# Optimization experiments

Hardware: AMD Instinct MI355X
Metric: run time of the kernel (lower is better)

Reference implementation:

```python
import jax, jax.numpy as jnp
import numpy as np

B, X_DIM, Z_DIM, K = 16384, 784, 64, 64
LOG2PI = 1.8378770664093453


def setup_inputs() -> dict:
    key = jax.random.key(0)
    ks = jax.random.split(key, 8)
    pi_raw = jax.random.uniform(ks[1], (B, K), dtype=jnp.float32) + 1e-3
    pi = pi_raw / jnp.sum(pi_raw, axis=1, keepdims=True)
    return {
        "x": jax.random.normal(ks[0], (B, X_DIM), dtype=jnp.float32),
        "pi": pi,
        "qz_mu": jax.random.normal(ks[2], (B, Z_DIM), dtype=jnp.float32),
        "qz_logsigma": 0.5 * jax.random.normal(ks[3], (B, Z_DIM), dtype=jnp.float32),
        "eps": jax.random.normal(ks[4], (B, Z_DIM), dtype=jnp.float32),
        "pz_y_mu": jax.random.normal(ks[5], (K, Z_DIM), dtype=jnp.float32),
        "pz_y_logsigma": jnp.zeros((K, Z_DIM), dtype=jnp.float32),  # log(init_sigma=1.0)
        "W_dec": jax.random.normal(ks[6], (Z_DIM, X_DIM), dtype=jnp.float32) / np.sqrt(Z_DIM),
        "b_dec": jnp.zeros((X_DIM,), dtype=jnp.float32),
    }


def reference(x, pi, qz_mu, qz_logsigma, eps, pz_y_mu, pz_y_logsigma, W_dec, b_dec):
    # GMMVAE.elbo with num_samples=1; rsample reparameterized with fixed eps.
    qs = jnp.exp(qz_logsigma)                      # [B, z]
    z = qz_mu + qs * eps                           # [B, z]

    # log p(x | z): unit-variance Gaussian likelihood with linear decoder
    mean = z @ W_dec + b_dec                       # [B, x]
    log_px_z = jnp.sum(-0.5 * (x - mean) ** 2 - 0.5 * LOG2PI)

    # py_z: vectorized over all k components (fuses the original Python loop)
    ps = jnp.exp(pz_y_logsigma)                    # [k, z]
    diff = z[:, None, :] - pz_y_mu[None, :, :]     # [B, k, z]
    comp_lp = jnp.sum(-0.5 * (diff / ps[None]) ** 2 - pz_y_logsigma[None] - 0.5 * LOG2PI, axis=-1)  # [B, k]
    log_pi = jnp.log(pi)
    pzy = comp_lp + log_pi                         # [B, k]
    log_py_z = pzy - jax.scipy.special.logsumexp(pzy, axis=1, keepdims=True)
    probs = jnp.exp(log_py_z)                      # [B, k]

    # kl_y = sum_b KL(Cat(py_z) || Cat(pi))
    kl_y = jnp.sum(probs * (log_py_z - log_pi))

    # kl_z = sum_b sum_k probs[b,k] * KL(N(qz_mu, qs) || N(mu_k, ps_k)).sum(z)
    mdiff = qz_mu[:, None, :] - pz_y_mu[None, :, :]  # [B, k, z]
    klz_bk = jnp.sum(
        pz_y_logsigma[None] - qz_logsigma[:, None, :]
        + (qs[:, None, :] ** 2 + mdiff ** 2) / (2.0 * ps[None] ** 2)
        - 0.5,
        axis=-1,
    )                                              # [B, k]
    kl_z = jnp.sum(probs * klz_bk)

    elbo = (log_px_z - kl_y - kl_z) / x.shape[0]
    return elbo
```

## Files before the change

### kernel.cpp

```cpp
#include <hip/hip_runtime.h>

#define NB 16384
#define XD 784
#define ZD 64
#define KK 64
#define LOG2PI_F 1.8378770664093453f
#define LDA 72

typedef __attribute__((ext_vector_type(8))) short short8;
typedef __attribute__((ext_vector_type(4))) float floatx4;


__device__ __forceinline__ float wave_sum(float x) {
    #pragma unroll
    for (int o = 32; o > 0; o >>= 1) x += __shfl_xor(x, o, 64);
    return x;
}

__device__ __forceinline__ unsigned short f2bf(float f) {
    unsigned u = __float_as_uint(f);
    unsigned r = (u + 0x7FFF + ((u >> 16) & 1)) >> 16;
    return (unsigned short)r;
}

__device__ __forceinline__ unsigned int pack2(float a, float b) {
    return (unsigned int)f2bf(a) | ((unsigned int)f2bf(b) << 16);
}

__global__ __launch_bounds__(256) void prep_kernel(
    const float* __restrict__ W, unsigned short* __restrict__ Wt)
{
    int idx = blockIdx.x * 256 + threadIdx.x;
    if (idx < ZD * XD) {
        int k = idx / XD;
        int n = idx - k * XD;
        Wt[n * ZD + k] = f2bf(W[idx]);
    }
}

__global__ __launch_bounds__(256) void mixture_mfma_kernel(
    const float* __restrict__ pi, const float* __restrict__ qmu,
    const float* __restrict__ qls, const float* __restrict__ eps,
    const float* __restrict__ pmu_g, const float* __restrict__ plog_g,
    float* __restrict__ kly_p, float* __restrict__ klz_p)
{
    __shared__ unsigned short Az2[64 * LDA];
    __shared__ unsigned short Azm[64 * LDA];
    __shared__ unsigned short Aq2[64 * LDA];
    __shared__ unsigned short Aqm[64 * LDA];
    __shared__ unsigned short Bi2[64 * LDA];
    __shared__ unsigned short Bm1[64 * LDA];
    __shared__ float Ck_s[KK], Sk_s[KK], Gk_s[KK], sq_s[64];
    __shared__ float r1[4], r2[4];

    const int tid  = threadIdx.x;
    const int row0 = blockIdx.x * 64;

    {
        const int r  = tid >> 2;
        const int q  = tid & 3;
        const int v0 = q * 16;
        const int gb = (row0 + r) * 64 + v0;
        float4 mu4[4], ls4[4], ep4[4];
        #pragma unroll
        for (int i = 0; i < 4; ++i) {
            mu4[i] = *(const float4*)&qmu[gb + 4 * i];
            ls4[i] = *(const float4*)&qls[gb + 4 * i];
            ep4[i] = *(const float4*)&eps[gb + 4 * i];
        }
        float sls = 0.f;
        unsigned int* pz2 = (unsigned int*)&Az2[r * LDA + v0];
        unsigned int* pzm = (unsigned int*)&Azm[r * LDA + v0];
        unsigned int* pq2 = (unsigned int*)&Aq2[r * LDA + v0];
        unsigned int* pqm = (unsigned int*)&Aqm[r * LDA + v0];
        #pragma unroll
        for (int i = 0; i < 4; ++i) {
            float m0[4] = {mu4[i].x, mu4[i].y, mu4[i].z, mu4[i].w};
            float l0[4] = {ls4[i].x, ls4[i].y, ls4[i].z, ls4[i].w};
            float e0[4] = {ep4[i].x, ep4[i].y, ep4[i].z, ep4[i].w};
            float z[4], q2[4];
            #pragma unroll
            for (int j = 0; j < 4; ++j) {
                float qs = __expf(l0[j]);
                z[j]  = fmaf(qs, e0[j], m0[j]);
                q2[j] = fmaf(m0[j], m0[j], qs * qs);
                sls += l0[j];
            }
            pz2[i * 2 + 0] = pack2(z[0] * z[0], z[1] * z[1]);
            pz2[i * 2 + 1] = pack2(z[2] * z[2], z[3] * z[3]);
            pzm[i * 2 + 0] = pack2(-2.f * z[0], -2.f * z[1]);
            pzm[i * 2 + 1] = pack2(-2.f * z[2], -2.f * z[3]);
            pq2[i * 2 + 0] = pack2(q2[0], q2[1]);
            pq2[i * 2 + 1] = pack2(q2[2], q2[3]);
            pqm[i * 2 + 0] = pack2(-2.f * m0[0], -2.f * m0[1]);
            pqm[i * 2 + 1] = pack2(-2.f * m0[2], -2.f * m0[3]);
        }
        sls += __shfl_xor(sls, 1, 64);
        sls += __shfl_xor(sls, 2, 64);
        if (q == 0) sq_s[r] = sls;
    }

    {
        const int k  = tid >> 2;
        const int q  = tid & 3;
        const int v0 = q * 16;
        const int gb = k * 64 + v0;
        float s = 0.f, g = 0.f;
        unsigned int* pi2 = (unsigned int*)&Bi2[k * LDA + v0];
        unsigned int* pm1 = (unsigned int*)&Bm1[k * LDA + v0];
        #pragma unroll
        for (int i = 0; i < 4; ++i) {
            float4 mu4 = *(const float4*)&pmu_g[gb + 4 * i];
            float4 lg4 = *(const float4*)&plog_g[gb + 4 * i];
            float m0[4] = {mu4.x, mu4.y, mu4.z, mu4.w};
            float l0[4] = {lg4.x, lg4.y, lg4.z, lg4.w};
            float i2v[4], m1v[4];
            #pragma unroll
            for (int j = 0; j < 4; ++j) {
                float i2 = 0.5f * __expf(-2.f * l0[j]);
                i2v[j] = i2;
                m1v[j] = m0[j] * i2;
                g = fmaf(m0[j] * m0[j], i2, g);
                s += l0[j];
            }
            pi2[i * 2 + 0] = pack2(i2v[0], i2v[1]);
            pi2[i * 2 + 1] = pack2(i2v[2], i2v[3]);
            pm1[i * 2 + 0] = pack2(m1v[0], m1v[1]);
            pm1[i * 2 + 1] = pack2(m1v[2], m1v[3]);
        }
        s += __shfl_xor(s, 1, 64);
        s += __shfl_xor(s, 2, 64);
        g += __shfl_xor(g, 1, 64);
        g += __shfl_xor(g, 2, 64);
        if (q == 0) {
            Sk_s[k] = s;
            Gk_s[k] = g;
            Ck_s[k] = -s - 32.0f * LOG2PI_F;
        }
    }
    __syncthreads();

    const int lane  = tid & 63;
    const int wid   = tid >> 6;
    const int mm    = lane & 15;
    const int quad  = lane >> 4;
    const int rbase = wid * 16;

    const short8 az2_0 = *(const short8*)&Az2[(rbase + mm) * LDA + quad * 8];
    const short8 az2_1 = *(const short8*)&Az2[(rbase + mm) * LDA + 32 + quad * 8];
    const short8 azm_0 = *(const short8*)&Azm[(rbase + mm) * LDA + quad * 8];
    const short8 azm_1 = *(const short8*)&Azm[(rbase + mm) * LDA + 32 + quad * 8];
    const short8 aq2_0 = *(const short8*)&Aq2[(rbase + mm) * LDA + quad * 8];
    const short8 aq2_1 = *(const short8*)&Aq2[(rbase + mm) * LDA + 32 + quad * 8];
    const short8 aqm_0 = *(const short8*)&Aqm[(rbase + mm) * LDA + quad * 8];
    const short8 aqm_1 = *(const short8*)&Aqm[(rbase + mm) * LDA + 32 + quad * 8];

    floatx4 acc_a[4], acc_c[4];
    #pragma unroll
    for (int t = 0; t < 4; ++t) {
        const int kr = t * 16 + mm;
        const short8 bi0 = *(const short8*)&Bi2[kr * LDA + quad * 8];
        const short8 bi1 = *(const short8*)&Bi2[kr * LDA + 32 + quad * 8];
        const short8 bm0 = *(const short8*)&Bm1[kr * LDA + quad * 8];
        const short8 bm1 = *(const short8*)&Bm1[kr * LDA + 32 + quad * 8];
        floatx4 ca = {0.f, 0.f, 0.f, 0.f};
        ca = __builtin_amdgcn_mfma_f32_16x16x32_bf16(az2_0, bi0, ca, 0, 0, 0);
        ca = __builtin_amdgcn_mfma_f32_16x16x32_bf16(az2_1, bi1, ca, 0, 0, 0);
        ca = __builtin_amdgcn_mfma_f32_16x16x32_bf16(azm_0, bm0, ca, 0, 0, 0);
        ca = __builtin_amdgcn_mfma_f32_16x16x32_bf16(azm_1, bm1, ca, 0, 0, 0);
        acc_a[t] = ca;
        floatx4 cc = {0.f, 0.f, 0.f, 0.f};
        cc = __builtin_amdgcn_mfma_f32_16x16x32_bf16(aq2_0, bi0, cc, 0, 0, 0);
        cc = __builtin_amdgcn_mfma_f32_16x16x32_bf16(aq2_1, bi1, cc, 0, 0, 0);
        cc = __builtin_amdgcn_mfma_f32_16x16x32_bf16(aqm_0, bm0, cc, 0, 0, 0);
        cc = __builtin_amdgcn_mfma_f32_16x16x32_bf16(aqm_1, bm1, cc, 0, 0, 0);
        acc_c[t] = cc;
    }

    float comp[4][4], pz[4][4];
    #pragma unroll
    for (int t = 0; t < 4; ++t) {
        const int k = t * 16 + mm;
        const float ck = Ck_s[k], gk = Gk_s[k];
        #pragma unroll
        for (int r = 0; r < 4; ++r) {
            const int gb = row0 + rbase + quad * 4 + r;
            comp[t][r] = ck - (acc_a[t][r] + gk);
            pz[t][r] = comp[t][r] + __logf(pi[gb * 64 + k]);
        }
    }

    float kly = 0.f, klz = 0.f;
    #pragma unroll
    for (int r = 0; r < 4; ++r) {
        float mx = fmaxf(fmaxf(pz[0][r], pz[1][r]), fmaxf(pz[2][r], pz[3][r]));
        #pragma unroll
        for (int o = 1; o <= 8; o <<= 1) mx = fmaxf(mx, __shfl_xor(mx, o, 64));
        float e[4];
        float s = 0.f;
        #pragma unroll
        for (int t = 0; t < 4; ++t) { e[t] = __expf(pz[t][r] - mx); s += e[t]; }
        #pragma unroll
        for (int o = 1; o <= 8; o <<= 1) s += __shfl_xor(s, o, 64);
        const float lse = mx + __logf(s);
        const float inv = __frcp_rn(s);
        const float sql = sq_s[rbase + quad * 4 + r];
        #pragma unroll
        for (int t = 0; t < 4; ++t) {
            const int k = t * 16 + mm;
            const float p = e[t] * inv;
            kly = fmaf(p, comp[t][r] - lse, kly);
            const float cv = acc_c[t][r] + Gk_s[k];
            klz = fmaf(p, Sk_s[k] - sql + cv - 32.0f, klz);
        }
    }

    kly = wave_sum(kly);
    klz = wave_sum(klz);
    if (lane == 0) { r1[wid] = kly; r2[wid] = klz; }
    __syncthreads();
    if (tid == 0) {
        kly_p[blockIdx.x] = r1[0] + r1[1] + r1[2] + r1[3];
        klz_p[blockIdx.x] = r2[0] + r2[1] + r2[2] + r2[3];
    }
}

__global__ __launch_bounds__(256) void decoder_mfma_kernel(
    const float* __restrict__ x, const float* __restrict__ qmu,
    const float* __restrict__ qls, const float* __restrict__ eps,
    const unsigned short* __restrict__ Wt, const float* __restrict__ bd,
    float* __restrict__ dec_p)
{
    __shared__ unsigned short zt[16 * 64];
    __shared__ float rs[4];
    const int tid  = threadIdx.x;
    const int row0 = blockIdx.x * 16;

    for (int i = tid; i < 16 * 64; i += 256) {
        int g = row0 * 64 + i;
        float z = fmaf(__expf(qls[g]), eps[g], qmu[g]);
        zt[i] = f2bf(z);
    }
    __syncthreads();

    const int lane = tid & 63;
    const int wid  = tid >> 6;
    const int m    = lane & 15;
    const int quad = lane >> 4;

    const short8 af0 = *(const short8*)&zt[m * 64 + quad * 8];
    const short8 af1 = *(const short8*)&zt[m * 64 + 32 + quad * 8];

    const int xrow = (row0 + quad * 4) * XD;

    float xa0, xa1, xa2, xa3, bb;
    short8 w0, w1;
    {
        const int col = wid * 16 + m;
        xa0 = x[xrow + 0 * XD + col];
        xa1 = x[xrow + 1 * XD + col];
        xa2 = x[xrow + 2 * XD + col];
        xa3 = x[xrow + 3 * XD + col];
        bb  = bd[col];
        w0  = *(const short8*)&Wt[col * 64 + quad * 8];
        w1  = *(const short8*)&Wt[col * 64 + 32 + quad * 8];
    }

    float accl = 0.f;
    #pragma unroll 1
    for (int t = wid; t < 49; t += 4) {
        const float cx0 = xa0, cx1 = xa1, cx2 = xa2, cx3 = xa3, cb = bb;
        const short8 cw0 = w0, cw1 = w1;
        const int tn = t + 4;
        if (tn < 49) {
            const int col = tn * 16 + m;
            xa0 = x[xrow + 0 * XD + col];
            xa1 = x[xrow + 1 * XD + col];
            xa2 = x[xrow + 2 * XD + col];
            xa3 = x[xrow + 3 * XD + col];
            bb  = bd[col];
            w0  = *(const short8*)&Wt[col * 64 + quad * 8];
            w1  = *(const short8*)&Wt[col * 64 + 32 + quad * 8];
        }
        floatx4 c = {0.f, 0.f, 0.f, 0.f};
        c = __builtin_amdgcn_mfma_f32_16x16x32_bf16(af0, cw0, c, 0, 0, 0);
        c = __builtin_amdgcn_mfma_f32_16x16x32_bf16(af1, cw1, c, 0, 0, 0);
        float d0 = cx0 - (c[0] + cb);
        float d1 = cx1 - (c[1] + cb);
        float d2 = cx2 - (c[2] + cb);
        float d3 = cx3 - (c[3] + cb);
        accl = fmaf(d0, d0, accl);
        accl = fmaf(d1, d1, accl);
        accl = fmaf(d2, d2, accl);
        accl = fmaf(d3, d3, accl);
    }

    float s = wave_sum(accl);
    if (lane == 0) rs[wid] = s;
    __syncthreads();
    if (tid == 0)
        dec_p[blockIdx.x] = -0.5f * (rs[0] + rs[1] + rs[2] + rs[3]);
}

__global__ __launch_bounds__(256) void finalize_kernel(
    const float* __restrict__ dec_p, const float* __restrict__ kly_p,
    const float* __restrict__ klz_p, float* __restrict__ out)
{
    __shared__ double s0[256], s1[256], s2[256];
    const int tid = threadIdx.x;
    double a0 = 0.0, a1 = 0.0, a2 = 0.0;
    for (int i = tid; i < 1024; i += 256) a0 += (double)dec_p[i];
    a1 = (double)kly_p[tid];
    a2 = (double)klz_p[tid];
    s0[tid] = a0; s1[tid] = a1; s2[tid] = a2;
    __syncthreads();
    #pragma unroll
    for (int off = 128; off > 0; off >>= 1) {
        if (tid < off) {
            s0[tid] += s0[tid + off];
            s1[tid] += s1[tid + off];
            s2[tid] += s2[tid + off];
        }
        __syncthreads();
    }
    if (tid == 0) {
        double lpx = s0[0] - 0.5 * 1.8378770664093453 * (double)NB * (double)XD;
        out[0] = (float)((lpx - s1[0] - s2[0]) / (double)NB);
    }
}

extern "C" void kernel_launch(void* const* d_in, const int* in_sizes, int n_in,
                              void* d_out, int out_size, void* d_ws, size_t ws_size,
                              hipStream_t stream) {
    const float* x    = (const float*)d_in[0];
    const float* pi   = (const float*)d_in[1];
    const float* qmu  = (const float*)d_in[2];
    const float* qls  = (const float*)d_in[3];
    const float* eps  = (const float*)d_in[4];
    const float* pmu  = (const float*)d_in[5];
    const float* plog = (const float*)d_in[6];
    const float* W    = (const float*)d_in[7];
    const float* bd   = (const float*)d_in[8];
    float* out = (float*)d_out;

    unsigned short* Wt = (unsigned short*)d_ws;
    float* fp    = (float*)((char*)d_ws + 100352);
    float* dec_p = fp;
    float* kly_p = fp + 1024;
    float* klz_p = fp + 1280;

    prep_kernel<<<(ZD * XD + 255) / 256, 256, 0, stream>>>(W, Wt);
    mixture_mfma_kernel<<<NB / 64, 256, 0, stream>>>(pi, qmu, qls, eps, pmu, plog, kly_p, klz_p);
    decoder_mfma_kernel<<<NB / 16, 256, 0, stream>>>(x, qmu, qls, eps, Wt, bd, dec_p);
    finalize_kernel<<<1, 256, 0, stream>>>(dec_p, kly_p, klz_p, out);
}
```

Before: 127.4 us.

## Fuse mixture KL and decoder kernels into one 16-row-per-block kernel

Merges the mixture (KL) kernel and the decoder likelihood kernel into a single kernel that processes 16 rows per block. The z, q and mu operands are computed once and shared through LDS, which avoids reloading qmu, qls and eps and saves a launch. Per-component prior terms are now precomputed once in prep_kernel and read from global memory, instead of being recomputed by every block. Each wave now handles 16 components, so the logsumexp is combined across waves through shared memory, which adds a barrier and extra exp calls.

```diff
diff --git a/kernel.cpp b/kernel.cpp
--- a/kernel.cpp
+++ b/kernel.cpp
@@ -28,86 +28,27 @@
 }
 
 __global__ __launch_bounds__(256) void prep_kernel(
-    const float* __restrict__ W, unsigned short* __restrict__ Wt)
+    const float* __restrict__ W, const float* __restrict__ pmu_g,
+    const float* __restrict__ plog_g,
+    unsigned short* __restrict__ Wt, unsigned short* __restrict__ Bi2_g,
+    unsigned short* __restrict__ Bm1_g, float* __restrict__ Sk_g,
+    float* __restrict__ Gk_g, float* __restrict__ Ck_g)
 {
-    int idx = blockIdx.x * 256 + threadIdx.x;
-    if (idx < ZD * XD) {
+    const int tid = threadIdx.x;
+    const int b = blockIdx.x;
+    if (b < 196) {
+        int idx = b * 256 + tid;
         int k = idx / XD;
         int n = idx - k * XD;
         Wt[n * ZD + k] = f2bf(W[idx]);
-    }
-}
-
-__global__ __launch_bounds__(256) void mixture_mfma_kernel(
-    const float* __restrict__ pi, const float* __restrict__ qmu,
-    const float* __restrict__ qls, const float* __restrict__ eps,
-    const float* __restrict__ pmu_g, const float* __restrict__ plog_g,
-    float* __restrict__ kly_p, float* __restrict__ klz_p)
-{
-    __shared__ unsigned short Az2[64 * LDA];
-    __shared__ unsigned short Azm[64 * LDA];
-    __shared__ unsigned short Aq2[64 * LDA];
-    __shared__ unsigned short Aqm[64 * LDA];
-    __shared__ unsigned short Bi2[64 * LDA];
-    __shared__ unsigned short Bm1[64 * LDA];
-    __shared__ float Ck_s[KK], Sk_s[KK], Gk_s[KK], sq_s[64];
-    __shared__ float r1[4], r2[4];
-
-    const int tid  = threadIdx.x;
-    const int row0 = blockIdx.x * 64;
-
-    {
-        const int r  = tid >> 2;
-        const int q  = tid & 3;
-        const int v0 = q * 16;
-        const int gb = (row0 + r) * 64 + v0;
-        float4 mu4[4], ls4[4], ep4[4];
-        #pragma unroll
-        for (int i = 0; i < 4; ++i) {
-            mu4[i] = *(const float4*)&qmu[gb + 4 * i];
-            ls4[i] = *(const float4*)&qls[gb + 4 * i];
-            ep4[i] = *(const float4*)&eps[gb + 4 * i];
-        }
-        float sls = 0.f;
-        unsigned int* pz2 = (unsigned int*)&Az2[r * LDA + v0];
-        unsigned int* pzm = (unsigned int*)&Azm[r * LDA + v0];
-        unsigned int* pq2 = (unsigned int*)&Aq2[r * LDA + v0];
-        unsigned int* pqm = (unsigned int*)&Aqm[r * LDA + v0];
-        #pragma unroll
-        for (int i = 0; i < 4; ++i) {
-            float m0[4] = {mu4[i].x, mu4[i].y, mu4[i].z, mu4[i].w};
-            float l0[4] = {ls4[i].x, ls4[i].y, ls4[i].z, ls4[i].w};
-            float e0[4] = {ep4[i].x, ep4[i].y, ep4[i].z, ep4[i].w};
-            float z[4], q2[4];
-            #pragma unroll
-            for (int j = 0; j < 4; ++j) {
-                float qs = __expf(l0[j]);
-                z[j]  = fmaf(qs, e0[j], m0[j]);
-                q2[j] = fmaf(m0[j], m0[j], qs * qs);
-                sls += l0[j];
-            }
-            pz2[i * 2 + 0] = pack2(z[0] * z[0], z[1] * z[1]);
-            pz2[i * 2 + 1] = pack2(z[2] * z[2], z[3] * z[3]);
-            pzm[i * 2 + 0] = pack2(-2.f * z[0], -2.f * z[1]);
-            pzm[i * 2 + 1] = pack2(-2.f * z[2], -2.f * z[3]);
-            pq2[i * 2 + 0] = pack2(q2[0], q2[1]);
-            pq2[i * 2 + 1] = pack2(q2[2], q2[3]);
-            pqm[i * 2 + 0] = pack2(-2.f * m0[0], -2.f * m0[1]);
-            pqm[i * 2 + 1] = pack2(-2.f * m0[2], -2.f * m0[3]);
-        }
-        sls += __shfl_xor(sls, 1, 64);
-        sls += __shfl_xor(sls, 2, 64);
-        if (q == 0) sq_s[r] = sls;
-    }
-
-    {
-        const int k  = tid >> 2;
-        const int q  = tid & 3;
+    } else {
+        const int k = tid >> 2;
+        const int q = tid & 3;
         const int v0 = q * 16;
         const int gb = k * 64 + v0;
         float s = 0.f, g = 0.f;
-        unsigned int* pi2 = (unsigned int*)&Bi2[k * LDA + v0];
-        unsigned int* pm1 = (unsigned int*)&Bm1[k * LDA + v0];
+        unsigned int* pi2 = (unsigned int*)&Bi2_g[k * 64 + v0];
+        unsigned int* pm1 = (unsigned int*)&Bm1_g[k * 64 + v0];
         #pragma unroll
         for (int i = 0; i < 4; ++i) {
             float4 mu4 = *(const float4*)&pmu_g[gb + 4 * i];
@@ -133,130 +74,155 @@
         g += __shfl_xor(g, 1, 64);
         g += __shfl_xor(g, 2, 64);
         if (q == 0) {
-            Sk_s[k] = s;
-            Gk_s[k] = g;
-            Ck_s[k] = -s - 32.0f * LOG2PI_F;
+            Sk_g[k] = s;
+            Gk_g[k] = g;
+            Ck_g[k] = -s - 32.0f * LOG2PI_F;
+        }
+    }
+}
+
+__global__ __launch_bounds__(256) void fused_kernel(
+    const float* __restrict__ x, const float* __restrict__ pi,
+    const float* __restrict__ qmu, const float* __restrict__ qls,
+    const float* __restrict__ eps,
+    const unsigned short* __restrict__ Wt, const float* __restrict__ bd,
+    const unsigned short* __restrict__ Bi2_g, const unsigned short* __restrict__ Bm1_g,
+    const float* __restrict__ Sk_g, const float* __restrict__ Gk_g,
+    const float* __restrict__ Ck_g,
+    float* __restrict__ dec_p, float* __restrict__ kly_p, float* __restrict__ klz_p)
+{
+    __shared__ unsigned short Az[16 * LDA];
+    __shared__ unsigned short Az2[16 * LDA];
+    __shared__ unsigned short Azm[16 * LDA];
+    __shared__ unsigned short Aq2[16 * LDA];
+    __shared__ unsigned short Aqm[16 * LDA];
+    __shared__ float Sk_s[64], Gk_s[64], Ck_s[64], sql_s[16];
+    __shared__ float MxP[4][16], SxP[4][16];
+    __shared__ float r1[4], r2[4], rs[4];
+
+    const int tid = threadIdx.x;
+    const int row0 = blockIdx.x * 16;
+
+    {
+        const int r = tid >> 4;
+        const int c = (tid & 15) * 4;
+        const int gb = (row0 + r) * 64 + c;
+        float4 mu4 = *(const float4*)&qmu[gb];
+        float4 ls4 = *(const float4*)&qls[gb];
+        float4 ep4 = *(const float4*)&eps[gb];
+        float m0[4] = {mu4.x, mu4.y, mu4.z, mu4.w};
+        float l0[4] = {ls4.x, ls4.y, ls4.z, ls4.w};
+        float e0[4] = {ep4.x, ep4.y, ep4.z, ep4.w};
+        float z[4], q2[4], sls = 0.f;
+        #pragma unroll
+        for (int j = 0; j < 4; ++j) {
+            float qs = __expf(l0[j]);
+            z[j] = fmaf(qs, e0[j], m0[j]);
+            q2[j] = fmaf(m0[j], m0[j], qs * qs);
+            sls += l0[j];
+        }
+        unsigned* pa = (unsigned*)&Az[r * LDA + c];
+        pa[0] = pack2(z[0], z[1]);               pa[1] = pack2(z[2], z[3]);
+        unsigned* pb = (unsigned*)&Az2[r * LDA + c];
+        pb[0] = pack2(z[0] * z[0], z[1] * z[1]); pb[1] = pack2(z[2] * z[2], z[3] * z[3]);
+        unsigned* pc = (unsigned*)&Azm[r * LDA + c];
+        pc[0] = pack2(-2.f * z[0], -2.f * z[1]); pc[1] = pack2(-2.f * z[2], -2.f * z[3]);
+        unsigned* pd = (unsigned*)&Aq2[r * LDA + c];
+        pd[0] = pack2(q2[0], q2[1]);             pd[1] = pack2(q2[2], q2[3]);
+        unsigned* pe = (unsigned*)&Aqm[r * LDA + c];
+        pe[0] = pack2(-2.f * m0[0], -2.f * m0[1]); pe[1] = pack2(-2.f * m0[2], -2.f * m0[3]);
+        sls += __shfl_xor(sls, 1, 64);
+        sls += __shfl_xor(sls, 2, 64);
+        sls += __shfl_xor(sls, 4, 64);
+        sls += __shfl_xor(sls, 8, 64);
+        if ((tid & 15) == 0) sql_s[r] = sls;
+        if (tid < 64) {
+            Sk_s[tid] = Sk_g[tid];
+            Gk_s[tid] = Gk_g[tid];
+            Ck_s[tid] = Ck_g[tid];
         }
     }
     __syncthreads();
 
-    const int lane  = tid & 63;
-    const int wid   = tid >> 6;
-    const int mm    = lane & 15;
-    const int quad  = lane >> 4;
-    const int rbase = wid * 16;
-
-    const short8 az2_0 = *(const short8*)&Az2[(rbase + mm) * LDA + quad * 8];
-    const short8 az2_1 = *(const short8*)&Az2[(rbase + mm) * LDA + 32 + quad * 8];
-    const short8 azm_0 = *(const short8*)&Azm[(rbase + mm) * LDA + quad * 8];
-    const short8 azm_1 = *(const short8*)&Azm[(rbase + mm) * LDA + 32 + quad * 8];
-    const short8 aq2_0 = *(const short8*)&Aq2[(rbase + mm) * LDA + quad * 8];
-    const short8 aq2_1 = *(const short8*)&Aq2[(rbase + mm) * LDA + 32 + quad * 8];
-    const short8 aqm_0 = *(const short8*)&Aqm[(rbase + mm) * LDA + quad * 8];
-    const short8 aqm_1 = *(const short8*)&Aqm[(rbase + mm) * LDA + 32 + quad * 8];
-
-    floatx4 acc_a[4], acc_c[4];
-    #pragma unroll
-    for (int t = 0; t < 4; ++t) {
-        const int kr = t * 16 + mm;
-        const short8 bi0 = *(const short8*)&Bi2[kr * LDA + quad * 8];
-        const short8 bi1 = *(const short8*)&Bi2[kr * LDA + 32 + quad * 8];
-        const short8 bm0 = *(const short8*)&Bm1[kr * LDA + quad * 8];
-        const short8 bm1 = *(const short8*)&Bm1[kr * LDA + 32 + quad * 8];
-        floatx4 ca = {0.f, 0.f, 0.f, 0.f};
+    const int lane = tid & 63;
+    const int w    = tid >> 6;
+    const int m    = lane & 15;
+    const int quad = lane >> 4;
+    const int kk   = w * 16 + m;
+
+    floatx4 ca = {0.f, 0.f, 0.f, 0.f}, cc = {0.f, 0.f, 0.f, 0.f};
+    {
+        const short8 az2_0 = *(const short8*)&Az2[m * LDA + quad * 8];
+        const short8 az2_1 = *(const short8*)&Az2[m * LDA + 32 + quad * 8];
+        const short8 azm_0 = *(const short8*)&Azm[m * LDA + quad * 8];
+        const short8 azm_1 = *(const short8*)&Azm[m * LDA + 32 + quad * 8];
+        const short8 aq2_0 = *(const short8*)&Aq2[m * LDA + quad * 8];
+        const short8 aq2_1 = *(const short8*)&Aq2[m * LDA + 32 + quad * 8];
+        const short8 aqm_0 = *(const short8*)&Aqm[m * LDA + quad * 8];
+        const short8 aqm_1 = *(const short8*)&Aqm[m * LDA + 32 + quad * 8];
+        const short8 bi0 = *(const short8*)&Bi2_g[kk * 64 + quad * 8];
+        const short8 bi1 = *(const short8*)&Bi2_g[kk * 64 + 32 + quad * 8];
+        const short8 bm0 = *(const short8*)&Bm1_g[kk * 64 + quad * 8];
+        const short8 bm1 = *(const short8*)&Bm1_g[kk * 64 + 32 + quad * 8];
         ca = __builtin_amdgcn_mfma_f32_16x16x32_bf16(az2_0, bi0, ca, 0, 0, 0);
         ca = __builtin_amdgcn_mfma_f32_16x16x32_bf16(az2_1, bi1, ca, 0, 0, 0);
         ca = __builtin_amdgcn_mfma_f32_16x16x32_bf16(azm_0, bm0, ca, 0, 0, 0);
         ca = __builtin_amdgcn_mfma_f32_16x16x32_bf16(azm_1, bm1, ca, 0, 0, 0);
-        acc_a[t] = ca;
-        floatx4 cc = {0.f, 0.f, 0.f, 0.f};
         cc = __builtin_amdgcn_mfma_f32_16x16x32_bf16(aq2_0, bi0, cc, 0, 0, 0);
         cc = __builtin_amdgcn_mfma_f32_16x16x32_bf16(aq2_1, bi1, cc, 0, 0, 0);
         cc = __builtin_amdgcn_mfma_f32_16x16x32_bf16(aqm_0, bm0, cc, 0, 0, 0);
         cc = __builtin_amdgcn_mfma_f32_16x16x32_bf16(aqm_1, bm1, cc, 0, 0, 0);
-        acc_c[t] = cc;
-    }
-
-    float comp[4][4], pz[4][4];
+    }
+
+    const float ckv = Ck_s[kk], gkv = Gk_s[kk], skv = Sk_s[kk];
+    float comp[4], ev[4], mxw[4], sw[4];
     #pragma unroll
-    for (int t = 0; t < 4; ++t) {
-        const int k = t * 16 + mm;
-        const float ck = Ck_s[k], gk = Gk_s[k];
+    for (int r = 0; r < 4; ++r) {
+        comp[r] = ckv - (ca[r] + gkv);
+        float pzv = comp[r] + __logf(pi[(row0 + quad * 4 + r) * 64 + kk]);
+        float mx = pzv;
+        #pragma unroll
+        for (int o = 1; o <= 8; o <<= 1) mx = fmaxf(mx, __shfl_xor(mx, o, 64));
+        float e = __expf(pzv - mx);
+        float s = e;
+        #pragma unroll
+        for (int o = 1; o <= 8; o <<= 1) s += __shfl_xor(s, o, 64);
+        mxw[r] = mx; sw[r] = s; ev[r] = e;
+    }
+    if (m == 0) {
         #pragma unroll
         for (int r = 0; r < 4; ++r) {
-            const int gb = row0 + rbase + quad * 4 + r;
-            comp[t][r] = ck - (acc_a[t][r] + gk);
-            pz[t][r] = comp[t][r] + __logf(pi[gb * 64 + k]);
-        }
-    }
+            MxP[w][quad * 4 + r] = mxw[r];
+            SxP[w][quad * 4 + r] = sw[r];
+        }
+    }
+    __syncthreads();
 
     float kly = 0.f, klz = 0.f;
     #pragma unroll
     for (int r = 0; r < 4; ++r) {
-        float mx = fmaxf(fmaxf(pz[0][r], pz[1][r]), fmaxf(pz[2][r], pz[3][r]));
-        #pragma unroll
-        for (int o = 1; o <= 8; o <<= 1) mx = fmaxf(mx, __shfl_xor(mx, o, 64));
-        float e[4];
-        float s = 0.f;
-        #pragma unroll
-        for (int t = 0; t < 4; ++t) { e[t] = __expf(pz[t][r] - mx); s += e[t]; }
-        #pragma unroll
-        for (int o = 1; o <= 8; o <<= 1) s += __shfl_xor(s, o, 64);
-        const float lse = mx + __logf(s);
-        const float inv = __frcp_rn(s);
-        const float sql = sq_s[rbase + quad * 4 + r];
-        #pragma unroll
-        for (int t = 0; t < 4; ++t) {
-            const int k = t * 16 + mm;
-            const float p = e[t] * inv;
-            kly = fmaf(p, comp[t][r] - lse, kly);
-            const float cv = acc_c[t][r] + Gk_s[k];
-            klz = fmaf(p, Sk_s[k] - sql + cv - 32.0f, klz);
-        }
-    }
-
+        const int row = quad * 4 + r;
+        float g0 = MxP[0][row], g1 = MxP[1][row], g2 = MxP[2][row], g3 = MxP[3][row];
+        float gmx = fmaxf(fmaxf(g0, g1), fmaxf(g2, g3));
+        float st = SxP[0][row] * __expf(g0 - gmx) + SxP[1][row] * __expf(g1 - gmx)
+                 + SxP[2][row] * __expf(g2 - gmx) + SxP[3][row] * __expf(g3 - gmx);
+        float lse = gmx + __logf(st);
+        float p = ev[r] * __expf(mxw[r] - gmx) * __frcp_rn(st);
+        kly = fmaf(p, comp[r] - lse, kly);
+        klz = fmaf(p, skv - sql_s[row] + cc[r] + gkv - 32.0f, klz);
+    }
     kly = wave_sum(kly);
     klz = wave_sum(klz);
-    if (lane == 0) { r1[wid] = kly; r2[wid] = klz; }
-    __syncthreads();
-    if (tid == 0) {
-        kly_p[blockIdx.x] = r1[0] + r1[1] + r1[2] + r1[3];
-        klz_p[blockIdx.x] = r2[0] + r2[1] + r2[2] + r2[3];
-    }
-}
-
-__global__ __launch_bounds__(256) void decoder_mfma_kernel(
-    const float* __restrict__ x, const float* __restrict__ qmu,
-    const float* __restrict__ qls, const float* __restrict__ eps,
-    const unsigned short* __restrict__ Wt, const float* __restrict__ bd,
-    float* __restrict__ dec_p)
-{
-    __shared__ unsigned short zt[16 * 64];
-    __shared__ float rs[4];
-    const int tid  = threadIdx.x;
-    const int row0 = blockIdx.x * 16;
-
-    for (int i = tid; i < 16 * 64; i += 256) {
-        int g = row0 * 64 + i;
-        float z = fmaf(__expf(qls[g]), eps[g], qmu[g]);
-        zt[i] = f2bf(z);
-    }
-    __syncthreads();
-
-    const int lane = tid & 63;
-    const int wid  = tid >> 6;
-    const int m    = lane & 15;
-    const int quad = lane >> 4;
-
-    const short8 af0 = *(const short8*)&zt[m * 64 + quad * 8];
-    const short8 af1 = *(const short8*)&zt[m * 64 + 32 + quad * 8];
-
+    if (lane == 0) { r1[w] = kly; r2[w] = klz; }
+
+    const short8 af0 = *(const short8*)&Az[m * LDA + quad * 8];
+    const short8 af1 = *(const short8*)&Az[m * LDA + 32 + quad * 8];
     const int xrow = (row0 + quad * 4) * XD;
 
     float xa0, xa1, xa2, xa3, bb;
     short8 w0, w1;
     {
-        const int col = wid * 16 + m;
+        const int col = w * 16 + m;
         xa0 = x[xrow + 0 * XD + col];
         xa1 = x[xrow + 1 * XD + col];
         xa2 = x[xrow + 2 * XD + col];
@@ -268,7 +234,7 @@
 
     float accl = 0.f;
     #pragma unroll 1
-    for (int t = wid; t < 49; t += 4) {
+    for (int t = w; t < 49; t += 4) {
         const float cx0 = xa0, cx1 = xa1, cx2 = xa2, cx3 = xa3, cb = bb;
         const short8 cw0 = w0, cw1 = w1;
         const int tn = t + 4;
@@ -295,11 +261,14 @@
         accl = fmaf(d3, d3, accl);
     }
 
-    float s = wave_sum(accl);
-    if (lane == 0) rs[wid] = s;
+    float sdec = wave_sum(accl);
+    if (lane == 0) rs[w] = sdec;
     __syncthreads();
-    if (tid == 0)
+    if (tid == 0) {
         dec_p[blockIdx.x] = -0.5f * (rs[0] + rs[1] + rs[2] + rs[3]);
+        kly_p[blockIdx.x] = r1[0] + r1[1] + r1[2] + r1[3];
+        klz_p[blockIdx.x] = r2[0] + r2[1] + r2[2] + r2[3];
+    }
 }
 
 __global__ __launch_bounds__(256) void finalize_kernel(
@@ -309,9 +278,11 @@
     __shared__ double s0[256], s1[256], s2[256];
     const int tid = threadIdx.x;
     double a0 = 0.0, a1 = 0.0, a2 = 0.0;
-    for (int i = tid; i < 1024; i += 256) a0 += (double)dec_p[i];
-    a1 = (double)kly_p[tid];
-    a2 = (double)klz_p[tid];
+    for (int i = tid; i < 1024; i += 256) {
+        a0 += (double)dec_p[i];
+        a1 += (double)kly_p[i];
+        a2 += (double)klz_p[i];
+    }
     s0[tid] = a0; s1[tid] = a1; s2[tid] = a2;
     __syncthreads();
     #pragma unroll
@@ -343,14 +314,20 @@
     const float* bd   = (const float*)d_in[8];
     float* out = (float*)d_out;
 
-    unsigned short* Wt = (unsigned short*)d_ws;
-    float* fp    = (float*)((char*)d_ws + 100352);
-    float* dec_p = fp;
-    float* kly_p = fp + 1024;
-    float* klz_p = fp + 1280;
-
-    prep_kernel<<<(ZD * XD + 255) / 256, 256, 0, stream>>>(W, Wt);
-    mixture_mfma_kernel<<<NB / 64, 256, 0, stream>>>(pi, qmu, qls, eps, pmu, plog, kly_p, klz_p);
-    decoder_mfma_kernel<<<NB / 16, 256, 0, stream>>>(x, qmu, qls, eps, Wt, bd, dec_p);
+    char* wsb = (char*)d_ws;
+    unsigned short* Wt   = (unsigned short*)(wsb);
+    unsigned short* Bi2g = (unsigned short*)(wsb + 100352);
+    unsigned short* Bm1g = (unsigned short*)(wsb + 108544);
+    float* Skg   = (float*)(wsb + 116736);
+    float* Gkg   = (float*)(wsb + 116992);
+    float* Ckg   = (float*)(wsb + 117248);
+    float* dec_p = (float*)(wsb + 117504);
+    float* kly_p = (float*)(wsb + 121600);
+    float* klz_p = (float*)(wsb + 125696);
+
+    prep_kernel<<<197, 256, 0, stream>>>(W, pmu, plog, Wt, Bi2g, Bm1g, Skg, Gkg, Ckg);
+    fused_kernel<<<NB / 16, 256, 0, stream>>>(x, pi, qmu, qls, eps, Wt, bd,
+                                              Bi2g, Bm1g, Skg, Gkg, Ckg,
+                                              dec_p, kly_p, klz_p);
     finalize_kernel<<<1, 256, 0, stream>>>(dec_p, kly_p, klz_p, out);
 }
```

Measured after the change: 126.2 us. About the same (-1.0%).
